# Kernel tuning notes

Hardware: AMD Instinct MI355X
Metric: run time of the kernel (lower is better)

The kernel has to match this reference:

```python
import jax, jax.numpy as jnp
import numpy as np

NUM_HEADER = 8
DIM_HIDDEN = 512
DIM_HEADER = DIM_HIDDEN // NUM_HEADER


def setup_inputs() -> dict:
    key = jax.random.key(0)
    ks = jax.random.split(key, 11)
    B, S, D = 2, 4096, DIM_HIDDEN
    scale = 1.0 / np.sqrt(D)
    inp = {
        "q": jax.random.normal(ks[0], (B, S, D), jnp.float32),
        "k": jax.random.normal(ks[1], (B, S, D), jnp.float32),
        "v": jax.random.normal(ks[2], (B, S, D), jnp.float32),
        # nn.Linear weights are [out, in]; y = x @ W.T + b
        "Wq": jax.random.normal(ks[3], (D, D), jnp.float32) * scale,
        "bq": jax.random.normal(ks[4], (D,), jnp.float32) * scale,
        "Wk": jax.random.normal(ks[5], (D, D), jnp.float32) * scale,
        "bk": jax.random.normal(ks[6], (D,), jnp.float32) * scale,
        "Wv": jax.random.normal(ks[7], (D, D), jnp.float32) * scale,
        "bv": jax.random.normal(ks[8], (D,), jnp.float32) * scale,
        "Wo": jax.random.normal(ks[9], (D, D), jnp.float32) * scale,
        "bo": jax.random.normal(ks[10], (D,), jnp.float32) * scale,
    }
    return inp


def reference(q, k, v, Wq, bq, Wk, bk, Wv, bv, Wo, bo):
    B = q.shape[0]
    H, dh = NUM_HEADER, DIM_HEADER

    def proj(x, W, b):
        # [B,S,D] -> [B,H,S,dh]
        y = jnp.einsum('bsd,ed->bse', x, W) + b
        return y.reshape(B, -1, H, dh).transpose(0, 2, 1, 3)

    qh = proj(q, Wq, bq)
    kh = proj(k, Wk, bk)
    vh = proj(v, Wv, bv)

    scores = jnp.einsum('bhqd,bhkd->bhqk', qh, kh) / jnp.sqrt(jnp.float32(dh))
    attn = jax.nn.softmax(scores, axis=-1)
    ctx = jnp.einsum('bhqk,bhkd->bhqd', attn, vh)
    concat = ctx.transpose(0, 2, 1, 3).reshape(B, -1, H * dh)
    return jnp.einsum('bsd,ed->bse', concat, Wo) + bo
```

## Files before the change

### kernel.cpp

```cpp
#include <hip/hip_runtime.h>
#include <hip/hip_bf16.h>

typedef __attribute__((ext_vector_type(8))) short short8;
typedef __attribute__((ext_vector_type(4))) float f32x4;
typedef __attribute__((ext_vector_type(16))) float f32x16;
typedef __attribute__((ext_vector_type(4))) float f4v;

#define SEQ 4096
#define NBH 16
#define SCALE_Q 0.18033688011112042f

#define MFMA16(a, b, c) __builtin_amdgcn_mfma_f32_16x16x32_bf16(a, b, c, 0, 0, 0)
#define MFMA32(a, b, c) __builtin_amdgcn_mfma_f32_32x32x16_bf16(a, b, c, 0, 0, 0)

__device__ __forceinline__ short f2bf(float f) {
  union { float f; unsigned u; } x; x.f = f;
  unsigned r = x.u + 0x7FFFu + ((x.u >> 16) & 1u);
  return (short)(r >> 16);
}

__device__ __forceinline__ unsigned cvt_pk_bf16(float lo, float hi) {
  unsigned r;
  asm("v_cvt_pk_bf16_f32 %0, %1, %2" : "=v"(r) : "v"(lo), "v"(hi));
  return r;
}

__device__ __forceinline__ short8 cvt8(const float* __restrict__ src) {
  f4v v0 = *(const f4v*)src;
  f4v v1 = *(const f4v*)(src + 4);
  union { unsigned u[4]; short8 s; } r;
  r.u[0] = cvt_pk_bf16(v0[0], v0[1]);
  r.u[1] = cvt_pk_bf16(v0[2], v0[3]);
  r.u[2] = cvt_pk_bf16(v1[0], v1[1]);
  r.u[3] = cvt_pk_bf16(v1[2], v1[3]);
  return r.s;
}

__device__ __forceinline__ void gll16(const void* g, void* l) {
  __builtin_amdgcn_global_load_lds(
      (const __attribute__((address_space(1))) void*)g,
      (__attribute__((address_space(3))) void*)l, 16, 0, 0);
}

__device__ __forceinline__ void pswap(unsigned& a, unsigned& b) {
  asm volatile("v_permlane32_swap_b32 %0, %1" : "+v"(a), "+v"(b));
}

#define SBAR()                              \
  __builtin_amdgcn_sched_barrier(0);        \
  __builtin_amdgcn_s_barrier();             \
  __builtin_amdgcn_sched_barrier(0)

__global__ __launch_bounds__(256) void cvt_w(
    const float* __restrict__ w0, const float* __restrict__ w1,
    const float* __restrict__ w2, const float* __restrict__ w3,
    short* __restrict__ dst)
{
  int i = blockIdx.x * 256 + threadIdx.x;
  int m = i >> 15;
  int off = (i & 32767) * 8;
  const float* s = (m == 0) ? w0 : (m == 1) ? w1 : (m == 2) ? w2 : w3;
  *(short8*)(dst + (size_t)m * 262144 + off) = cvt8(s + off);
}

template <int MODE>
__global__ __launch_bounds__(256) void gemm_bt(
    const float* __restrict__ Af, const short* __restrict__ Ab,
    const short* __restrict__ Wb, const float* __restrict__ bias,
    const float* __restrict__ Opart, const float* __restrict__ lsum,
    void* __restrict__ Cout)
{
  __shared__ __align__(16) char smemA[64 * 72 * 2];
  __shared__ __align__(16) char smemB[128 * 64 * 2];
  short (*As)[72] = (short(*)[72])smemA;
  const int t    = threadIdx.x;
  const int lane = t & 63;
  const int w    = t >> 6;
  const int g    = lane >> 4;
  const int q    = lane & 15;
  const int tile_n = blockIdx.x * 128;
  const int tile_m = blockIdx.y * 64;

  f32x4 acc[4][2];
#pragma unroll
  for (int mi = 0; mi < 4; ++mi)
#pragma unroll
    for (int ni = 0; ni < 2; ++ni)
#pragma unroll
      for (int j = 0; j < 4; ++j) acc[mi][ni][j] = 0.f;

  for (int k0 = 0; k0 < 512; k0 += 64) {
    __syncthreads();
    if (MODE <= 2) {
#pragma unroll
      for (int it = 0; it < 2; ++it) {
        int i = it * 256 + t;
        int r = i >> 3, sg = i & 7;
        *(short8*)&As[r][sg * 8] =
            cvt8(Af + (size_t)(tile_m + r) * 512 + k0 + sg * 8);
      }
    } else if (MODE == 3) {
#pragma unroll
      for (int it = 0; it < 2; ++it) {
        int i = it * 256 + t;
        int row = i >> 3, cg = i & 7;
        const char* gp = (const char*)Ab +
            ((size_t)(tile_m + row) * 512 + k0) * 2 + ((cg ^ (row & 7)) << 4);
        gll16(gp, smemA + (size_t)(it * 256 + (t & ~63)) * 16);
      }
    } else {
#pragma unroll
      for (int it = 0; it < 2; ++it) {
        int i = it * 256 + t;
        int row = i >> 3, cg = i & 7;
        int cgs = cg ^ (row & 7);
        int m = tile_m + row;
        int b = m >> 12, s = m & 4095;
        int h = k0 >> 6;
        size_t g0 = (size_t)(b * 8 + h) * SEQ + s;
        float inv = 1.0f / (lsum[g0] + lsum[g0 + (size_t)NBH * SEQ]);
        const float* o0 = Opart + g0 * 64 + cgs * 8;
        const float* o1 = Opart + (g0 + (size_t)NBH * SEQ) * 64 + cgs * 8;
        f4v a0 = *(const f4v*)o0, a1 = *(const f4v*)(o0 + 4);
        f4v b0 = *(const f4v*)o1, b1 = *(const f4v*)(o1 + 4);
        float vv[8];
#pragma unroll
        for (int j = 0; j < 4; ++j) vv[j] = (a0[j] + b0[j]) * inv;
#pragma unroll
        for (int j = 0; j < 4; ++j) vv[4 + j] = (a1[j] + b1[j]) * inv;
        union { unsigned u[4]; short8 s8; } r;
        r.u[0] = cvt_pk_bf16(vv[0], vv[1]);
        r.u[1] = cvt_pk_bf16(vv[2], vv[3]);
        r.u[2] = cvt_pk_bf16(vv[4], vv[5]);
        r.u[3] = cvt_pk_bf16(vv[6], vv[7]);
        *(short8*)(smemA + (size_t)i * 16) = r.s8;
      }
    }
#pragma unroll
    for (int it = 0; it < 4; ++it) {
      int i = it * 256 + t;
      int row = i >> 3, cg = i & 7;
      const char* gp = (const char*)Wb +
          ((size_t)(tile_n + row) * 512 + k0) * 2 + ((cg ^ (row & 7)) << 4);
      gll16(gp, smemB + (size_t)(it * 256 + (t & ~63)) * 16);
    }
    __syncthreads();
#pragma unroll
    for (int kk = 0; kk < 2; ++kk) {
      short8 af[4], bfv[2];
#pragma unroll
      for (int mi = 0; mi < 4; ++mi) {
        int rA = mi * 16 + q;
        if (MODE <= 2)
          af[mi] = *(const short8*)&As[rA][kk * 32 + g * 8];
        else
          af[mi] = *(const short8*)(smemA + rA * 128 +
                                    (((4 * kk + g) ^ (rA & 7)) << 4));
      }
#pragma unroll
      for (int ni = 0; ni < 2; ++ni) {
        int rB = w * 32 + ni * 16 + q;
        bfv[ni] = *(const short8*)(smemB + rB * 128 +
                                   (((4 * kk + g) ^ (rB & 7)) << 4));
      }
#pragma unroll
      for (int mi = 0; mi < 4; ++mi)
#pragma unroll
        for (int ni = 0; ni < 2; ++ni) {
          if (MODE == 2)
            acc[mi][ni] = MFMA16(bfv[ni], af[mi], acc[mi][ni]);
          else
            acc[mi][ni] = MFMA16(af[mi], bfv[ni], acc[mi][ni]);
        }
    }
  }

#pragma unroll
  for (int mi = 0; mi < 4; ++mi) {
#pragma unroll
    for (int ni = 0; ni < 2; ++ni) {
#pragma unroll
      for (int j = 0; j < 4; ++j) {
        if (MODE == 2) {
          int e = tile_n + w * 32 + ni * 16 + 4 * g + j;
          int srow = tile_m + mi * 16 + q;
          float val = acc[mi][ni][j] + bias[e];
          int b = srow >> 12, sl = srow & 4095;
          int h = e >> 6, d = e & 63;
          ((short*)Cout)[((size_t)((b * 8 + h) * 64 + d)) * SEQ + sl] = f2bf(val);
        } else {
          int m = tile_m + mi * 16 + g * 4 + j;
          int e = tile_n + w * 32 + ni * 16 + q;
          float val = acc[mi][ni][j] + bias[e];
          if (MODE == 0) val *= SCALE_Q;
          if (MODE >= 3) {
            ((float*)Cout)[(size_t)m * 512 + e] = val;
          } else {
            int b = m >> 12, s = m & 4095;
            int h = e >> 6, d = e & 63;
            ((short*)Cout)[((size_t)(b * 8 + h) * SEQ + s) * 64 + d] = f2bf(val);
          }
        }
      }
    }
  }
}

template <int NSPLIT>
__global__ __launch_bounds__(256, 4) void attn_kernel(
    const short* __restrict__ Qh, const short* __restrict__ Kh,
    const short* __restrict__ Vt, short* __restrict__ ctx,
    float* __restrict__ Opart, float* __restrict__ lsum)
{
  __shared__ __align__(16) char smem[2][16384];
  const int t    = threadIdx.x;
  const int lane = t & 63;
  const int w    = t >> 6;
  const int l31  = lane & 31;
  const int hi   = lane >> 5;

  const int fid = blockIdx.x;
  int qt, bh, split;
  if (NSPLIT == 1) {
    int lid = (fid & 7) * 64 + (fid >> 3);
    qt = lid & 31; bh = lid >> 5; split = 0;
  } else {
    int lid = (fid & 7) * 128 + (fid >> 3);
    qt = lid & 31; split = (lid >> 5) & 1; bh = lid >> 6;
  }
  const int NT  = (SEQ / 64) / NSPLIT;
  const int kt0 = split * NT;

  const size_t kbase = (size_t)bh * SEQ * 64;
  const size_t vbase = (size_t)bh * 64 * SEQ;
  const int q0 = qt * 128 + w * 32;

  short8 qf[4];
#pragma unroll
  for (int m = 0; m < 4; ++m)
    qf[m] = *(const short8*)(Qh + kbase + (size_t)(q0 + l31) * 64 + m * 16 + hi * 8);

  f32x16 fz;
#pragma unroll
  for (int r = 0; r < 16; ++r) fz[r] = 0.f;
  f32x16 acc0 = fz, acc1 = fz;
  float lrun = 0.f;

  const int rif  = lane >> 3;
  const int scol = ((lane & 7) ^ rif) * 16;
  const int xr   = (hi * 16) ^ ((lane & 7) << 4);

#define STAGE(buf, kt)                                                         \
  {                                                                            \
    _Pragma("unroll")                                                          \
    for (int i = 0; i < 4; ++i) {                                              \
      int c = w * 4 + i;                                                       \
      char* ldst = &smem[buf][c * 1024];                                       \
      if (c < 8) {                                                             \
        int row = c * 8 + rif;                                                 \
        const char* gp = (const char*)Kh +                                     \
            ((kbase + (size_t)((kt) * 64 + row) * 64) * 2 + scol);             \
        gll16(gp, ldst);                                                       \
      } else {                                                                 \
        int row = (c - 8) * 8 + rif;                                           \
        const char* gp = (const char*)Vt +                                     \
            ((vbase + (size_t)row * SEQ + (kt) * 64) * 2 + scol);              \
        gll16(gp, ldst);                                                       \
      }                                                                        \
    }                                                                          \
  }

  STAGE(0, kt0);
  int cur = 0;

  for (int it = 0; it < NT; ++it) {
    const int kt = kt0 + it;
    if (it < NT - 1) {
      STAGE(cur ^ 1, kt + 1);
      asm volatile("s_waitcnt vmcnt(4)" ::: "memory");
    } else {
      asm volatile("s_waitcnt vmcnt(0)" ::: "memory");
    }
    SBAR();

    const char* Kb = &smem[cur][0];
    const char* Vb = &smem[cur][8192];

    f32x16 s0, s1;
    {
      short8 k0 = *(const short8*)(Kb + (size_t)(l31) * 128 + ((32 * 0) ^ xr));
      short8 k1 = *(const short8*)(Kb + (size_t)(32 + l31) * 128 + ((32 * 0) ^ xr));
      __builtin_amdgcn_s_setprio(1);
      s0 = MFMA32(k0, qf[0], fz);
      s1 = MFMA32(k1, qf[0], fz);
      __builtin_amdgcn_s_setprio(0);
    }
#pragma unroll
    for (int m = 1; m < 4; ++m) {
      short8 k0 = *(const short8*)(Kb + (size_t)(l31) * 128 + ((32 * m) ^ xr));
      short8 k1 = *(const short8*)(Kb + (size_t)(32 + l31) * 128 + ((32 * m) ^ xr));
      __builtin_amdgcn_s_setprio(1);
      s0 = MFMA32(k0, qf[m], s0);
      s1 = MFMA32(k1, qf[m], s1);
      __builtin_amdgcn_s_setprio(0);
    }

#pragma unroll
    for (int r = 0; r < 16; ++r) s0[r] = __builtin_amdgcn_exp2f(s0[r]);
    float rs0;
    {
      float b_[8];
#pragma unroll
      for (int r = 0; r < 8; ++r) b_[r] = s0[r] + s0[r + 8];
#pragma unroll
      for (int r = 0; r < 4; ++r) b_[r] += b_[r + 4];
      rs0 = (b_[0] + b_[1]) + (b_[2] + b_[3]);
    }
    union { unsigned u[4]; short8 v; } A0c, A1c;
    {
      unsigned p0 = cvt_pk_bf16(s0[0], s0[1]);
      unsigned p1 = cvt_pk_bf16(s0[2], s0[3]);
      unsigned p2 = cvt_pk_bf16(s0[4], s0[5]);
      unsigned p3 = cvt_pk_bf16(s0[6], s0[7]);
      unsigned p4 = cvt_pk_bf16(s0[8], s0[9]);
      unsigned p5 = cvt_pk_bf16(s0[10], s0[11]);
      unsigned p6 = cvt_pk_bf16(s0[12], s0[13]);
      unsigned p7 = cvt_pk_bf16(s0[14], s0[15]);
      pswap(p0, p2); pswap(p1, p3); pswap(p4, p6); pswap(p5, p7);
      A0c.u[0] = p0; A0c.u[1] = p1; A0c.u[2] = p2; A0c.u[3] = p3;
      A1c.u[0] = p4; A1c.u[1] = p5; A1c.u[2] = p6; A1c.u[3] = p7;
    }
#pragma unroll
    for (int h2 = 0; h2 < 2; ++h2) {
      short8 pa = h2 ? A1c.v : A0c.v;
      short8 vf0 = *(const short8*)(Vb + (size_t)(l31) * 128 + ((32 * h2) ^ xr));
      short8 vf1 = *(const short8*)(Vb + (size_t)(32 + l31) * 128 + ((32 * h2) ^ xr));
      __builtin_amdgcn_s_setprio(1);
      acc0 = MFMA32(pa, vf0, acc0);
      acc1 = MFMA32(pa, vf1, acc1);
      __builtin_amdgcn_s_setprio(0);
    }

#pragma unroll
    for (int r = 0; r < 16; ++r) s1[r] = __builtin_amdgcn_exp2f(s1[r]);
    float rs1;
    {
      float b_[8];
#pragma unroll
      for (int r = 0; r < 8; ++r) b_[r] = s1[r] + s1[r + 8];
#pragma unroll
      for (int r = 0; r < 4; ++r) b_[r] += b_[r + 4];
      rs1 = (b_[0] + b_[1]) + (b_[2] + b_[3]);
    }
    {
      unsigned p0 = cvt_pk_bf16(s1[0], s1[1]);
      unsigned p1 = cvt_pk_bf16(s1[2], s1[3]);
      unsigned p2 = cvt_pk_bf16(s1[4], s1[5]);
      unsigned p3 = cvt_pk_bf16(s1[6], s1[7]);
      unsigned p4 = cvt_pk_bf16(s1[8], s1[9]);
      unsigned p5 = cvt_pk_bf16(s1[10], s1[11]);
      unsigned p6 = cvt_pk_bf16(s1[12], s1[13]);
      unsigned p7 = cvt_pk_bf16(s1[14], s1[15]);
      pswap(p0, p2); pswap(p1, p3); pswap(p4, p6); pswap(p5, p7);
      A0c.u[0] = p0; A0c.u[1] = p1; A0c.u[2] = p2; A0c.u[3] = p3;
      A1c.u[0] = p4; A1c.u[1] = p5; A1c.u[2] = p6; A1c.u[3] = p7;
    }
#pragma unroll
    for (int h2 = 0; h2 < 2; ++h2) {
      short8 pa = h2 ? A1c.v : A0c.v;
      short8 vf0 = *(const short8*)(Vb + (size_t)(l31) * 128 + ((64 + 32 * h2) ^ xr));
      short8 vf1 = *(const short8*)(Vb + (size_t)(32 + l31) * 128 + ((64 + 32 * h2) ^ xr));
      __builtin_amdgcn_s_setprio(1);
      acc0 = MFMA32(pa, vf0, acc0);
      acc1 = MFMA32(pa, vf1, acc1);
      __builtin_amdgcn_s_setprio(0);
    }

    float rs = rs0 + rs1;
    rs += __shfl_xor(rs, 32);
    lrun += rs;

    SBAR();
    cur ^= 1;
  }

  if (NSPLIT == 1) {
    const int b = bh >> 3, hh = bh & 7;
    const float inv = 1.0f / lrun;
#pragma unroll
    for (int r = 0; r < 16; ++r) {
      int ql = (r & 3) + 8 * (r >> 2) + 4 * hi;
      float iv = __shfl(inv, ql);
      int qrow = q0 + ql;
      size_t off = ((size_t)(b * SEQ + qrow)) * 512 + hh * 64 + l31;
      ctx[off]      = f2bf(acc0[r] * iv);
      ctx[off + 32] = f2bf(acc1[r] * iv);
    }
  } else {
    float* Ob = Opart + (((size_t)(split * NBH + bh) * SEQ + q0)) * 64;
#pragma unroll
    for (int r = 0; r < 16; ++r) {
      int ql = (r & 3) + 8 * (r >> 2) + 4 * hi;
      Ob[(size_t)ql * 64 + l31]      = acc0[r];
      Ob[(size_t)ql * 64 + l31 + 32] = acc1[r];
    }
    if (hi == 0)
      lsum[(size_t)(split * NBH + bh) * SEQ + q0 + l31] = lrun;
  }
}

extern "C" void kernel_launch(void* const* d_in, const int* in_sizes, int n_in,
                              void* d_out, int out_size, void* d_ws, size_t ws_size,
                              hipStream_t stream) {
  const float* q  = (const float*)d_in[0];
  const float* k  = (const float*)d_in[1];
  const float* v  = (const float*)d_in[2];
  const float* Wq = (const float*)d_in[3];
  const float* bq = (const float*)d_in[4];
  const float* Wk = (const float*)d_in[5];
  const float* bk = (const float*)d_in[6];
  const float* Wv = (const float*)d_in[7];
  const float* bv = (const float*)d_in[8];
  const float* Wo = (const float*)d_in[9];
  const float* bo = (const float*)d_in[10];

  const size_t NELT = (size_t)NBH * SEQ * 64;
  short* Qh  = (short*)d_ws;
  short* Kh  = Qh + NELT;
  short* Vt  = Kh + NELT;
  short* ctx = Vt + NELT;
  short* Wb  = ctx + NELT;
  float* Opart = (float*)(Wb + 4 * 262144);
  float* lsum  = Opart + 2 * (size_t)NBH * SEQ * 64;
  const char* ws_end = (const char*)(lsum + 2 * (size_t)NBH * SEQ);
  const bool split2 = ws_size >= (size_t)(ws_end - (const char*)d_ws);

  dim3 tb(256);
  cvt_w<<<dim3(512), tb, 0, stream>>>(Wq, Wk, Wv, Wo, Wb);

  dim3 gb(4, 128);
  gemm_bt<0><<<gb, tb, 0, stream>>>(q, nullptr, Wb,          bq, nullptr, nullptr, (void*)Qh);
  gemm_bt<1><<<gb, tb, 0, stream>>>(k, nullptr, Wb + 262144, bk, nullptr, nullptr, (void*)Kh);
  gemm_bt<2><<<gb, tb, 0, stream>>>(v, nullptr, Wb + 524288, bv, nullptr, nullptr, (void*)Vt);
  if (split2) {
    attn_kernel<2><<<dim3(1024), tb, 0, stream>>>(Qh, Kh, Vt, ctx, Opart, lsum);
    gemm_bt<4><<<gb, tb, 0, stream>>>(nullptr, nullptr, Wb + 786432, bo, Opart, lsum, d_out);
  } else {
    attn_kernel<1><<<dim3(512), tb, 0, stream>>>(Qh, Kh, Vt, ctx, Opart, lsum);
    gemm_bt<3><<<gb, tb, 0, stream>>>(nullptr, ctx, Wb + 786432, bo, nullptr, nullptr, d_out);
  }
}
```

Measured before the change: 160.9 us.

## Batch Q/K/V projections into one launch and restructure attention double-buffer sync

Merges the three separate Q, K, V projection GEMM launches into a single kernel with a z grid dimension, so all 1536 blocks fill the GPU together and two launch gaps and tail effects go away. In the attention loop, the next tile's prefetch now starts after a full vmcnt(0) wait and barrier instead of before the wait, and the trailing barrier is removed. This uses one barrier per iteration but gives less overlap between the global loads and compute.

New measurement: 163.2 us. Within noise of the previous version (+1.4%).

```diff
diff --git a/kernel.cpp b/kernel.cpp
--- a/kernel.cpp
+++ b/kernel.cpp
@@ -63,16 +63,65 @@
   *(short8*)(dst + (size_t)m * 262144 + off) = cvt8(s + off);
 }
 
-template <int MODE>
-__global__ __launch_bounds__(256) void gemm_bt(
-    const float* __restrict__ Af, const short* __restrict__ Ab,
-    const short* __restrict__ Wb, const float* __restrict__ bias,
-    const float* __restrict__ Opart, const float* __restrict__ lsum,
-    void* __restrict__ Cout)
+template <bool SWAP>
+__device__ __forceinline__ void qkv_kloop(
+    const float* __restrict__ Af, const short* __restrict__ W,
+    char* smemA, char* smemB, f32x4 (&acc)[4][2],
+    int tile_m, int tile_n, int t, int g, int q, int w)
+{
+  short (*As)[72] = (short(*)[72])smemA;
+  for (int k0 = 0; k0 < 512; k0 += 64) {
+    __syncthreads();
+#pragma unroll
+    for (int it = 0; it < 2; ++it) {
+      int i = it * 256 + t;
+      int r = i >> 3, sg = i & 7;
+      *(short8*)&As[r][sg * 8] =
+          cvt8(Af + (size_t)(tile_m + r) * 512 + k0 + sg * 8);
+    }
+#pragma unroll
+    for (int it = 0; it < 4; ++it) {
+      int i = it * 256 + t;
+      int row = i >> 3, cg = i & 7;
+      const char* gp = (const char*)W +
+          ((size_t)(tile_n + row) * 512 + k0) * 2 + ((cg ^ (row & 7)) << 4);
+      gll16(gp, smemB + (size_t)(it * 256 + (t & ~63)) * 16);
+    }
+    __syncthreads();
+#pragma unroll
+    for (int kk = 0; kk < 2; ++kk) {
+      short8 af[4], bfv[2];
+#pragma unroll
+      for (int mi = 0; mi < 4; ++mi)
+        af[mi] = *(const short8*)&As[mi * 16 + q][kk * 32 + g * 8];
+#pragma unroll
+      for (int ni = 0; ni < 2; ++ni) {
+        int rB = w * 32 + ni * 16 + q;
+        bfv[ni] = *(const short8*)(smemB + rB * 128 +
+                                   (((4 * kk + g) ^ (rB & 7)) << 4));
+      }
+#pragma unroll
+      for (int mi = 0; mi < 4; ++mi)
+#pragma unroll
+        for (int ni = 0; ni < 2; ++ni) {
+          if (SWAP)
+            acc[mi][ni] = MFMA16(bfv[ni], af[mi], acc[mi][ni]);
+          else
+            acc[mi][ni] = MFMA16(af[mi], bfv[ni], acc[mi][ni]);
+        }
+    }
+  }
+}
+
+__global__ __launch_bounds__(256) void qkv_gemm(
+    const float* __restrict__ qin, const float* __restrict__ kin,
+    const float* __restrict__ vin, const short* __restrict__ Wb,
+    const float* __restrict__ bq, const float* __restrict__ bk,
+    const float* __restrict__ bv,
+    short* __restrict__ Qh, short* __restrict__ Kh, short* __restrict__ Vt)
 {
   __shared__ __align__(16) char smemA[64 * 72 * 2];
   __shared__ __align__(16) char smemB[128 * 64 * 2];
-  short (*As)[72] = (short(*)[72])smemA;
   const int t    = threadIdx.x;
   const int lane = t & 63;
   const int w    = t >> 6;
@@ -80,6 +129,69 @@
   const int q    = lane & 15;
   const int tile_n = blockIdx.x * 128;
   const int tile_m = blockIdx.y * 64;
+  const int z      = blockIdx.z;
+
+  const float* Af   = (z == 0) ? qin : (z == 1) ? kin : vin;
+  const float* bias = (z == 0) ? bq  : (z == 1) ? bk  : bv;
+  const short* W    = Wb + (size_t)z * 262144;
+
+  f32x4 acc[4][2];
+#pragma unroll
+  for (int mi = 0; mi < 4; ++mi)
+#pragma unroll
+    for (int ni = 0; ni < 2; ++ni)
+#pragma unroll
+      for (int j = 0; j < 4; ++j) acc[mi][ni][j] = 0.f;
+
+  if (z == 2)
+    qkv_kloop<true>(Af, W, smemA, smemB, acc, tile_m, tile_n, t, g, q, w);
+  else
+    qkv_kloop<false>(Af, W, smemA, smemB, acc, tile_m, tile_n, t, g, q, w);
+
+#pragma unroll
+  for (int mi = 0; mi < 4; ++mi) {
+#pragma unroll
+    for (int ni = 0; ni < 2; ++ni) {
+#pragma unroll
+      for (int j = 0; j < 4; ++j) {
+        if (z == 2) {
+          int e = tile_n + w * 32 + ni * 16 + 4 * g + j;
+          int srow = tile_m + mi * 16 + q;
+          float val = acc[mi][ni][j] + bias[e];
+          int b = srow >> 12, sl = srow & 4095;
+          int h = e >> 6, d = e & 63;
+          Vt[((size_t)((b * 8 + h) * 64 + d)) * SEQ + sl] = f2bf(val);
+        } else {
+          int m = tile_m + mi * 16 + g * 4 + j;
+          int e = tile_n + w * 32 + ni * 16 + q;
+          float val = acc[mi][ni][j] + bias[e];
+          int b = m >> 12, s = m & 4095;
+          int h = e >> 6, d = e & 63;
+          size_t off = ((size_t)(b * 8 + h) * SEQ + s) * 64 + d;
+          if (z == 0) Qh[off] = f2bf(val * SCALE_Q);
+          else        Kh[off] = f2bf(val);
+        }
+      }
+    }
+  }
+}
+
+template <int MODE>
+__global__ __launch_bounds__(256) void gemm_bt(
+    const short* __restrict__ Ab,
+    const short* __restrict__ Wb, const float* __restrict__ bias,
+    const float* __restrict__ Opart, const float* __restrict__ lsum,
+    void* __restrict__ Cout)
+{
+  __shared__ __align__(16) char smemA[64 * 72 * 2];
+  __shared__ __align__(16) char smemB[128 * 64 * 2];
+  const int t    = threadIdx.x;
+  const int lane = t & 63;
+  const int w    = t >> 6;
+  const int g    = lane >> 4;
+  const int q    = lane & 15;
+  const int tile_n = blockIdx.x * 128;
+  const int tile_m = blockIdx.y * 64;
 
   f32x4 acc[4][2];
 #pragma unroll
@@ -91,15 +203,7 @@
 
   for (int k0 = 0; k0 < 512; k0 += 64) {
     __syncthreads();
-    if (MODE <= 2) {
-#pragma unroll
-      for (int it = 0; it < 2; ++it) {
-        int i = it * 256 + t;
-        int r = i >> 3, sg = i & 7;
-        *(short8*)&As[r][sg * 8] =
-            cvt8(Af + (size_t)(tile_m + r) * 512 + k0 + sg * 8);
-      }
-    } else if (MODE == 3) {
+    if (MODE == 3) {
 #pragma unroll
       for (int it = 0; it < 2; ++it) {
         int i = it * 256 + t;
@@ -151,11 +255,8 @@
 #pragma unroll
       for (int mi = 0; mi < 4; ++mi) {
         int rA = mi * 16 + q;
-        if (MODE <= 2)
-          af[mi] = *(const short8*)&As[rA][kk * 32 + g * 8];
-        else
-          af[mi] = *(const short8*)(smemA + rA * 128 +
-                                    (((4 * kk + g) ^ (rA & 7)) << 4));
+        af[mi] = *(const short8*)(smemA + rA * 128 +
+                                  (((4 * kk + g) ^ (rA & 7)) << 4));
       }
 #pragma unroll
       for (int ni = 0; ni < 2; ++ni) {
@@ -166,12 +267,8 @@
 #pragma unroll
       for (int mi = 0; mi < 4; ++mi)
 #pragma unroll
-        for (int ni = 0; ni < 2; ++ni) {
-          if (MODE == 2)
-            acc[mi][ni] = MFMA16(bfv[ni], af[mi], acc[mi][ni]);
-          else
-            acc[mi][ni] = MFMA16(af[mi], bfv[ni], acc[mi][ni]);
-        }
+        for (int ni = 0; ni < 2; ++ni)
+          acc[mi][ni] = MFMA16(af[mi], bfv[ni], acc[mi][ni]);
     }
   }
 
@@ -181,26 +278,9 @@
     for (int ni = 0; ni < 2; ++ni) {
 #pragma unroll
       for (int j = 0; j < 4; ++j) {
-        if (MODE == 2) {
-          int e = tile_n + w * 32 + ni * 16 + 4 * g + j;
-          int srow = tile_m + mi * 16 + q;
-          float val = acc[mi][ni][j] + bias[e];
-          int b = srow >> 12, sl = srow & 4095;
-          int h = e >> 6, d = e & 63;
-          ((short*)Cout)[((size_t)((b * 8 + h) * 64 + d)) * SEQ + sl] = f2bf(val);
-        } else {
-          int m = tile_m + mi * 16 + g * 4 + j;
-          int e = tile_n + w * 32 + ni * 16 + q;
-          float val = acc[mi][ni][j] + bias[e];
-          if (MODE == 0) val *= SCALE_Q;
-          if (MODE >= 3) {
-            ((float*)Cout)[(size_t)m * 512 + e] = val;
-          } else {
-            int b = m >> 12, s = m & 4095;
-            int h = e >> 6, d = e & 63;
-            ((short*)Cout)[((size_t)(b * 8 + h) * SEQ + s) * 64 + d] = f2bf(val);
-          }
-        }
+        int m = tile_m + mi * 16 + g * 4 + j;
+        int e = tile_n + w * 32 + ni * 16 + q;
+        ((float*)Cout)[(size_t)m * 512 + e] = acc[mi][ni][j] + bias[e];
       }
     }
   }
@@ -275,13 +355,9 @@
 
   for (int it = 0; it < NT; ++it) {
     const int kt = kt0 + it;
-    if (it < NT - 1) {
-      STAGE(cur ^ 1, kt + 1);
-      asm volatile("s_waitcnt vmcnt(4)" ::: "memory");
-    } else {
-      asm volatile("s_waitcnt vmcnt(0)" ::: "memory");
-    }
+    asm volatile("s_waitcnt vmcnt(0)" ::: "memory");
     SBAR();
+    if (it < NT - 1) STAGE(cur ^ 1, kt + 1);
 
     const char* Kb = &smem[cur][0];
     const char* Vb = &smem[cur][8192];
@@ -380,7 +456,6 @@
     rs += __shfl_xor(rs, 32);
     lrun += rs;
 
-    SBAR();
     cur ^= 1;
   }
 
@@ -438,15 +513,13 @@
   dim3 tb(256);
   cvt_w<<<dim3(512), tb, 0, stream>>>(Wq, Wk, Wv, Wo, Wb);
 
-  dim3 gb(4, 128);
-  gemm_bt<0><<<gb, tb, 0, stream>>>(q, nullptr, Wb,          bq, nullptr, nullptr, (void*)Qh);
-  gemm_bt<1><<<gb, tb, 0, stream>>>(k, nullptr, Wb + 262144, bk, nullptr, nullptr, (void*)Kh);
-  gemm_bt<2><<<gb, tb, 0, stream>>>(v, nullptr, Wb + 524288, bv, nullptr, nullptr, (void*)Vt);
+  qkv_gemm<<<dim3(4, 128, 3), tb, 0, stream>>>(q, k, v, Wb, bq, bk, bv,
+                                               Qh, Kh, Vt);
   if (split2) {
     attn_kernel<2><<<dim3(1024), tb, 0, stream>>>(Qh, Kh, Vt, ctx, Opart, lsum);
-    gemm_bt<4><<<gb, tb, 0, stream>>>(nullptr, nullptr, Wb + 786432, bo, Opart, lsum, d_out);
+    gemm_bt<4><<<dim3(4, 128), tb, 0, stream>>>(nullptr, Wb + 786432, bo, Opart, lsum, d_out);
   } else {
     attn_kernel<1><<<dim3(512), tb, 0, stream>>>(Qh, Kh, Vt, ctx, Opart, lsum);
-    gemm_bt<3><<<gb, tb, 0, stream>>>(nullptr, ctx, Wb + 786432, bo, nullptr, nullptr, d_out);
-  }
-}
+    gemm_bt<3><<<dim3(4, 128), tb, 0, stream>>>(ctx, Wb + 786432, bo, nullptr, nullptr, d_out);
+  }
+}
```
